# Kernel optimization log

Hardware: AMD Instinct MI355X
Metric: run time of the kernel (lower is better)

The kernel has to match this reference:

```python
import jax, jax.numpy as jnp
import numpy as np

B, Fch, H, W, K = 16, 6, 512, 512, 8
ITERS = 12
TEMP = 0.15
EPS = 1e-6


def setup_inputs() -> dict:
    key = jax.random.key(0)
    k1, k2 = jax.random.split(key)
    feat = jax.random.normal(k1, (B, Fch, H, W), dtype=jnp.float32)
    idx = jax.random.randint(k2, (B, K), 0, H * W)
    return {"feat": feat, "idx": idx}


def reference(feat, idx):
    Bn, F_, Hh, Ww = feat.shape
    N = Hh * Ww
    # (B,F,H,W) -> (B,N,F), per-channel standardize over pixels (torch std is unbiased)
    X = feat.reshape(Bn, F_, N).transpose(0, 2, 1)
    X = X - X.mean(axis=1, keepdims=True)
    X = X / jnp.clip(X.std(axis=1, keepdims=True, ddof=1), EPS, None)
    # initial centroids: gather K random pixels per batch
    C0 = jnp.take_along_axis(X, idx[:, :, None], axis=1)  # (B,K,F)
    x2 = jnp.sum(X * X, axis=2, keepdims=True)  # (B,N,1), loop-invariant

    def step(carry, _):
        C, _S = carry
        c2 = jnp.sum(C * C, axis=2)[:, None, :]            # (B,1,K)
        xc = jnp.einsum('bnf,bkf->bnk', X, C)              # (B,N,K)
        d2 = jnp.clip(x2 + c2 - 2.0 * xc, 0.0, None)
        S = jax.nn.softmax(-d2 / TEMP, axis=2)             # (B,N,K)
        denom = jnp.clip(S.sum(axis=1)[:, :, None], EPS, None)  # (B,K,1)
        Cn = jnp.einsum('bnk,bnf->bkf', S, X) / denom
        return (Cn, S), None

    S_init = jnp.zeros((Bn, N, K), dtype=feat.dtype)
    (_, S), _ = jax.lax.scan(step, (C0, S_init), None, length=ITERS)
    # last S (computed from centroids of the previous update), as in the torch loop
    S_img = S.transpose(0, 2, 1).reshape(Bn, K, Hh, Ww)
    S_img = S_img / jnp.clip(S_img.sum(axis=1, keepdims=True), EPS, None)
    return S_img
```

## Files before the change

kernel.cpp:

```cpp
#include <hip/hip_runtime.h>
#include <math.h>

#define Bn    16
#define FCH   6
#define NPIX  262144
#define KC    8
#define NITERS 12
#define EPSF  1e-6f
#define ALPHA2 19.235933878519512f

#if __has_builtin(__builtin_amdgcn_exp2f)
#define EXP2(x) __builtin_amdgcn_exp2f(x)
#else
#define EXP2(x) __expf((x) * 0.6931471805599453f)
#endif

#if __has_builtin(__builtin_amdgcn_rcpf)
#define RCPF(x) __builtin_amdgcn_rcpf(x)
#else
#define RCPF(x) (1.0f / (x))
#endif

#define WS_SCALE 0
#define WS_SHIFT 96
#define WS_C     192
#define WS_PART  2048
#define WS_PART2 5120
#define WS_ACC0  8192
#define ACCBUF_STRIDE 1024

#define TPB 256
#define PPT 32

__device__ __forceinline__ float rfl(float x) {
    return __int_as_float(__builtin_amdgcn_readfirstlane(__float_as_int(x)));
}

__global__ __launch_bounds__(256) void stats_partial(const float* __restrict__ feat,
                                                     float* __restrict__ ws) {
    const int bf = blockIdx.x >> 5;
    const int c  = blockIdx.x & 31;
    const float4* p = (const float4*)(feat + (size_t)bf * NPIX) + c * 2048;
    float s = 0.f, ss = 0.f;
    for (int i = threadIdx.x; i < 2048; i += 256) {
        float4 v = p[i];
        s  += v.x + v.y + v.z + v.w;
        ss += v.x * v.x + v.y * v.y + v.z * v.z + v.w * v.w;
    }
#pragma unroll
    for (int off = 32; off > 0; off >>= 1) {
        s  += __shfl_down(s,  off, 64);
        ss += __shfl_down(ss, off, 64);
    }
    __shared__ float sh[8];
    const int w = threadIdx.x >> 6;
    if ((threadIdx.x & 63) == 0) { sh[w] = s; sh[4 + w] = ss; }
    __syncthreads();
    if (threadIdx.x == 0) {
        s  = sh[0] + sh[1] + sh[2] + sh[3];
        ss = sh[4] + sh[5] + sh[6] + sh[7];
        ws[WS_PART  + blockIdx.x] = s;
        ws[WS_PART2 + blockIdx.x] = ss;
    }
}

__global__ void init_kernel(const float* __restrict__ feat,
                            const int* __restrict__ idx,
                            float* __restrict__ ws) {
    const int t = threadIdx.x;
    for (int i = t; i < ACCBUF_STRIDE; i += 128) ws[WS_ACC0 + i] = 0.f;
    if (t < Bn * FCH) {
        float s = 0.f, ss = 0.f;
        for (int c = 0; c < 32; ++c) {
            s  += ws[WS_PART  + t * 32 + c];
            ss += ws[WS_PART2 + t * 32 + c];
        }
        float mean = s / (float)NPIX;
        float var  = (ss - s * mean) / (float)(NPIX - 1);
        float sd   = sqrtf(fmaxf(var, 0.f));
        float scale = 1.f / fmaxf(sd, EPSF);
        ws[WS_SCALE + t] = scale;
        ws[WS_SHIFT + t] = -mean * scale;
    }
    __syncthreads();
    {
        const int b = t / KC;
        const int n = idx[t];
        for (int f = 0; f < FCH; ++f) {
            const int bf = b * FCH + f;
            float v = fmaf(feat[(size_t)bf * NPIX + n], ws[WS_SCALE + bf], ws[WS_SHIFT + bf]);
            ws[WS_C + t * FCH + f] = v;
        }
    }
}

template <int LAST>
__global__ __launch_bounds__(TPB, 2) void assign_kernel(const float* __restrict__ feat,
                                                        const float* __restrict__ ws,
                                                        float* __restrict__ out,
                                                        float* __restrict__ accAdd,
                                                        const float* __restrict__ accRead,
                                                        float* __restrict__ accZero,
                                                        const int first) {
    const int b = blockIdx.y;
    const int t = threadIdx.x;

    __shared__ float sWb[KC * FCH + KC];
    __shared__ float sBlk[KC * FCH + KC];

    if (t < KC) {
        float sc[FCH], sh[FCH], C[FCH];
#pragma unroll
        for (int f = 0; f < FCH; ++f) {
            sc[f] = ws[WS_SCALE + b * FCH + f];
            sh[f] = ws[WS_SHIFT + b * FCH + f];
        }
        if (first) {
#pragma unroll
            for (int f = 0; f < FCH; ++f) C[f] = ws[WS_C + (b * KC + t) * FCH + f];
        } else {
            float as  = accRead[b * 64 + 48 + t];
            float inv = 1.f / fmaxf(as, EPSF);
#pragma unroll
            for (int f = 0; f < FCH; ++f)
                C[f] = (sc[f] * accRead[b * 64 + t * FCH + f] + sh[f] * as) * inv;
        }
        float c2 = 0.f, sd = 0.f;
#pragma unroll
        for (int f = 0; f < FCH; ++f) {
            c2 = fmaf(C[f], C[f], c2);
            sd = fmaf(sh[f], C[f], sd);
            sWb[t * FCH + f] = ALPHA2 * sc[f] * C[f];
        }
        sWb[KC * FCH + t] = ALPHA2 * sd - 0.5f * ALPHA2 * c2;
    }
    if (!LAST) {
        if (t < KC * FCH + KC) sBlk[t] = 0.f;
        if (blockIdx.x == 0 && t < 64) accZero[b * 64 + t] = 0.f;
    }
    __syncthreads();

    float W[KC][FCH], bias[KC];
#pragma unroll
    for (int k = 0; k < KC; ++k) {
        bias[k] = rfl(sWb[KC * FCH + k]);
#pragma unroll
        for (int f = 0; f < FCH; ++f) W[k][f] = rfl(sWb[k * FCH + f]);
    }

    const float4* fb4 = (const float4*)(feat + (size_t)b * FCH * NPIX);
    const int base4 = blockIdx.x * (PPT * TPB / 4) + t;

    float accC[KC][FCH], accS[KC];
    if (!LAST) {
#pragma unroll
        for (int k = 0; k < KC; ++k) {
            accS[k] = 0.f;
#pragma unroll
            for (int f = 0; f < FCH; ++f) accC[k][f] = 0.f;
        }
    }

    float4 cur[FCH];
#pragma unroll
    for (int f = 0; f < FCH; ++f) cur[f] = fb4[f * (NPIX / 4) + base4];

    for (int j = 0; j < PPT / 4; ++j) {
        float4 nxt[FCH];
        {
            const int jn = (j + 1 < PPT / 4) ? (j + 1) : j;
            const int i4n = base4 + jn * TPB;
#pragma unroll
            for (int f = 0; f < FCH; ++f) nxt[f] = fb4[f * (NPIX / 4) + i4n];
        }

        float rr[FCH][4];
#pragma unroll
        for (int f = 0; f < FCH; ++f) {
            rr[f][0] = cur[f].x; rr[f][1] = cur[f].y; rr[f][2] = cur[f].z; rr[f][3] = cur[f].w;
        }
        float sv[KC][4];
#pragma unroll
        for (int px = 0; px < 4; ++px) {
            float l[KC];
#pragma unroll
            for (int k = 0; k < KC; ++k) {
                float v = bias[k];
#pragma unroll
                for (int f = 0; f < FCH; ++f) v = fmaf(rr[f][px], W[k][f], v);
                l[k] = v;
            }
            float m01 = fmaxf(l[0], l[1]), m23 = fmaxf(l[2], l[3]);
            float m45 = fmaxf(l[4], l[5]), m67 = fmaxf(l[6], l[7]);
            float m = fmaxf(fmaxf(m01, m23), fmaxf(m45, m67));
            float e[KC];
#pragma unroll
            for (int k = 0; k < KC; ++k) e[k] = EXP2(l[k] - m);
            float s01 = e[0] + e[1], s23 = e[2] + e[3];
            float s45 = e[4] + e[5], s67 = e[6] + e[7];
            float sum = (s01 + s23) + (s45 + s67);
            const float inv = RCPF(sum);
            if (LAST) {
#pragma unroll
                for (int k = 0; k < KC; ++k) sv[k][px] = e[k] * inv;
            } else {
#pragma unroll
                for (int k = 0; k < KC; ++k) {
                    float s = e[k] * inv;
                    accS[k] += s;
#pragma unroll
                    for (int f = 0; f < FCH; ++f) accC[k][f] = fmaf(s, rr[f][px], accC[k][f]);
                }
            }
        }
        if (LAST) {
            const int i4 = base4 + j * TPB;
            float4* out4 = (float4*)out;
#pragma unroll
            for (int k = 0; k < KC; ++k)
                out4[((size_t)(b * KC + k)) * (NPIX / 4) + i4] =
                    make_float4(sv[k][0], sv[k][1], sv[k][2], sv[k][3]);
        }

#pragma unroll
        for (int f = 0; f < FCH; ++f) cur[f] = nxt[f];
    }

    if (!LAST) {
#pragma unroll
        for (int k = 0; k < KC; ++k) {
#pragma unroll
            for (int off = 32; off > 0; off >>= 1) accS[k] += __shfl_down(accS[k], off, 64);
#pragma unroll
            for (int f = 0; f < FCH; ++f)
#pragma unroll
                for (int off = 32; off > 0; off >>= 1) accC[k][f] += __shfl_down(accC[k][f], off, 64);
        }
        if ((t & 63) == 0) {
#pragma unroll
            for (int k = 0; k < KC; ++k) {
                atomicAdd(&sBlk[KC * FCH + k], accS[k]);
#pragma unroll
                for (int f = 0; f < FCH; ++f) atomicAdd(&sBlk[k * FCH + f], accC[k][f]);
            }
        }
        __syncthreads();
        if (t < KC * FCH)
            atomicAdd(&accAdd[b * 64 + t], sBlk[t]);
        else if (t < KC * FCH + KC)
            atomicAdd(&accAdd[b * 64 + 48 + (t - KC * FCH)], sBlk[t]);
    }
}

extern "C" void kernel_launch(void* const* d_in, const int* in_sizes, int n_in,
                              void* d_out, int out_size, void* d_ws, size_t ws_size,
                              hipStream_t stream) {
    const float* feat = (const float*)d_in[0];
    const int*   idx  = (const int*)d_in[1];
    float* out = (float*)d_out;
    float* ws  = (float*)d_ws;

    stats_partial<<<Bn * FCH * 32, 256, 0, stream>>>(feat, ws);
    init_kernel<<<1, 128, 0, stream>>>(feat, idx, ws);

    dim3 grid(NPIX / (PPT * TPB), Bn);
    for (int it = 0; it < NITERS; ++it) {
        float*       bufA = ws + WS_ACC0 + (it % 3)       * ACCBUF_STRIDE;
        const float* bufR = ws + WS_ACC0 + ((it + 2) % 3) * ACCBUF_STRIDE;
        float*       bufZ = ws + WS_ACC0 + ((it + 1) % 3) * ACCBUF_STRIDE;
        if (it == NITERS - 1)
            assign_kernel<1><<<grid, TPB, 0, stream>>>(feat, ws, out, nullptr, bufR, nullptr, 0);
        else
            assign_kernel<0><<<grid, TPB, 0, stream>>>(feat, ws, out, bufA, bufR, bufZ, it == 0);
    }
}
```

Before: 547.5 us.

## Fuse all k-means passes into one persistent cooperative kernel with grid syncs

Replaces the sequence of stats, init and twelve assign-kernel launches with a single cooperative kernel of 512 blocks. The phases are separated by grid-wide barriers, and cross-block data goes through relaxed agent-scope atomics. The aim is to remove per-launch overhead and the gaps between the 14 launches. The cost is grid.sync barriers plus fences, and an occupancy limit of 2 blocks per CU. If the cooperative launch fails, the code falls back to the old multi-kernel path.

```diff
diff --git a/kernel.cpp b/kernel.cpp
--- a/kernel.cpp
+++ b/kernel.cpp
@@ -1,5 +1,8 @@
 #include <hip/hip_runtime.h>
+#include <hip/hip_cooperative_groups.h>
 #include <math.h>
+
+namespace cg = cooperative_groups;
 
 #define Bn    16
 #define FCH   6
@@ -31,9 +34,281 @@
 
 #define TPB 256
 #define PPT 32
+#define NBLK 512
 
 __device__ __forceinline__ float rfl(float x) {
     return __int_as_float(__builtin_amdgcn_readfirstlane(__float_as_int(x)));
+}
+
+__device__ __forceinline__ float ald(const float* p) {
+    return __hip_atomic_load(p, __ATOMIC_RELAXED, __HIP_MEMORY_SCOPE_AGENT);
+}
+__device__ __forceinline__ void ast(float* p, float v) {
+    __hip_atomic_store(p, v, __ATOMIC_RELAXED, __HIP_MEMORY_SCOPE_AGENT);
+}
+
+template <int LAST>
+__device__ __forceinline__ void pass_body(const float4* __restrict__ fb4,
+                                          float* __restrict__ out,
+                                          float* __restrict__ accAdd,
+                                          const float (&W)[KC][FCH],
+                                          const float (&bias)[KC],
+                                          float* __restrict__ sBlk,
+                                          const int b, const int bx, const int t) {
+    const int base4 = bx * (PPT * TPB / 4) + t;
+
+    float accC[KC][FCH], accS[KC];
+    if (!LAST) {
+#pragma unroll
+        for (int k = 0; k < KC; ++k) {
+            accS[k] = 0.f;
+#pragma unroll
+            for (int f = 0; f < FCH; ++f) accC[k][f] = 0.f;
+        }
+    }
+
+    float4 cur[FCH];
+#pragma unroll
+    for (int f = 0; f < FCH; ++f) cur[f] = fb4[f * (NPIX / 4) + base4];
+
+    for (int j = 0; j < PPT / 4; ++j) {
+        float4 nxt[FCH];
+        {
+            const int jn = (j + 1 < PPT / 4) ? (j + 1) : j;
+            const int i4n = base4 + jn * TPB;
+#pragma unroll
+            for (int f = 0; f < FCH; ++f) nxt[f] = fb4[f * (NPIX / 4) + i4n];
+        }
+
+        float rr[FCH][4];
+#pragma unroll
+        for (int f = 0; f < FCH; ++f) {
+            rr[f][0] = cur[f].x; rr[f][1] = cur[f].y; rr[f][2] = cur[f].z; rr[f][3] = cur[f].w;
+        }
+        float sv[KC][4];
+#pragma unroll
+        for (int px = 0; px < 4; ++px) {
+            float l[KC];
+#pragma unroll
+            for (int k = 0; k < KC; ++k) {
+                float v = bias[k];
+#pragma unroll
+                for (int f = 0; f < FCH; ++f) v = fmaf(rr[f][px], W[k][f], v);
+                l[k] = v;
+            }
+            float m01 = fmaxf(l[0], l[1]), m23 = fmaxf(l[2], l[3]);
+            float m45 = fmaxf(l[4], l[5]), m67 = fmaxf(l[6], l[7]);
+            float m = fmaxf(fmaxf(m01, m23), fmaxf(m45, m67));
+            float e[KC];
+#pragma unroll
+            for (int k = 0; k < KC; ++k) e[k] = EXP2(l[k] - m);
+            float s01 = e[0] + e[1], s23 = e[2] + e[3];
+            float s45 = e[4] + e[5], s67 = e[6] + e[7];
+            float sum = (s01 + s23) + (s45 + s67);
+            const float inv = RCPF(sum);
+            if (LAST) {
+#pragma unroll
+                for (int k = 0; k < KC; ++k) sv[k][px] = e[k] * inv;
+            } else {
+#pragma unroll
+                for (int k = 0; k < KC; ++k) {
+                    float s = e[k] * inv;
+                    accS[k] += s;
+#pragma unroll
+                    for (int f = 0; f < FCH; ++f) accC[k][f] = fmaf(s, rr[f][px], accC[k][f]);
+                }
+            }
+        }
+        if (LAST) {
+            const int i4 = base4 + j * TPB;
+            float4* out4 = (float4*)out;
+#pragma unroll
+            for (int k = 0; k < KC; ++k)
+                out4[((size_t)(b * KC + k)) * (NPIX / 4) + i4] =
+                    make_float4(sv[k][0], sv[k][1], sv[k][2], sv[k][3]);
+        }
+
+#pragma unroll
+        for (int f = 0; f < FCH; ++f) cur[f] = nxt[f];
+    }
+
+    if (!LAST) {
+#pragma unroll
+        for (int k = 0; k < KC; ++k) {
+#pragma unroll
+            for (int off = 32; off > 0; off >>= 1) accS[k] += __shfl_down(accS[k], off, 64);
+#pragma unroll
+            for (int f = 0; f < FCH; ++f)
+#pragma unroll
+                for (int off = 32; off > 0; off >>= 1) accC[k][f] += __shfl_down(accC[k][f], off, 64);
+        }
+        if ((t & 63) == 0) {
+#pragma unroll
+            for (int k = 0; k < KC; ++k) {
+                atomicAdd(&sBlk[KC * FCH + k], accS[k]);
+#pragma unroll
+                for (int f = 0; f < FCH; ++f) atomicAdd(&sBlk[k * FCH + f], accC[k][f]);
+            }
+        }
+        __syncthreads();
+        if (t < KC * FCH)
+            atomicAdd(&accAdd[b * 64 + t], sBlk[t]);
+        else if (t < KC * FCH + KC)
+            atomicAdd(&accAdd[b * 64 + 48 + (t - KC * FCH)], sBlk[t]);
+    }
+}
+
+__device__ __forceinline__ void build_Wb_coh(const float* __restrict__ ws,
+                                             const float* __restrict__ accRead,
+                                             float* __restrict__ sWb,
+                                             const int b, const int t, const int first) {
+    if (t < KC) {
+        float sc[FCH], sh[FCH], C[FCH];
+#pragma unroll
+        for (int f = 0; f < FCH; ++f) {
+            sc[f] = ald(&ws[WS_SCALE + b * FCH + f]);
+            sh[f] = ald(&ws[WS_SHIFT + b * FCH + f]);
+        }
+        if (first) {
+#pragma unroll
+            for (int f = 0; f < FCH; ++f) C[f] = ald(&ws[WS_C + (b * KC + t) * FCH + f]);
+        } else {
+            float as  = ald(&accRead[b * 64 + 48 + t]);
+            float inv = 1.f / fmaxf(as, EPSF);
+#pragma unroll
+            for (int f = 0; f < FCH; ++f)
+                C[f] = (sc[f] * ald(&accRead[b * 64 + t * FCH + f]) + sh[f] * as) * inv;
+        }
+        float c2 = 0.f, sd = 0.f;
+#pragma unroll
+        for (int f = 0; f < FCH; ++f) {
+            c2 = fmaf(C[f], C[f], c2);
+            sd = fmaf(sh[f], C[f], sd);
+            sWb[t * FCH + f] = ALPHA2 * sc[f] * C[f];
+        }
+        sWb[KC * FCH + t] = ALPHA2 * sd - 0.5f * ALPHA2 * c2;
+    }
+}
+
+__global__ __launch_bounds__(TPB, 2) void fused_kernel(const float* __restrict__ feat,
+                                                       const int* __restrict__ idx,
+                                                       float* __restrict__ out,
+                                                       float* __restrict__ ws) {
+    cg::grid_group grid = cg::this_grid();
+    const int bid = blockIdx.x;
+    const int t   = threadIdx.x;
+
+    __shared__ float shr[8];
+    __shared__ float sWb[KC * FCH + KC];
+    __shared__ float sBlk[KC * FCH + KC];
+
+    if (bid == 0)
+        for (int i = t; i < ACCBUF_STRIDE; i += TPB) ast(&ws[WS_ACC0 + i], 0.f);
+
+    for (int task = bid; task < Bn * FCH * 32; task += NBLK) {
+        const int bf = task >> 5;
+        const int c  = task & 31;
+        const float4* p = (const float4*)(feat + (size_t)bf * NPIX) + c * 2048;
+        float s = 0.f, ss = 0.f;
+        for (int i = t; i < 2048; i += TPB) {
+            float4 v = p[i];
+            s  += v.x + v.y + v.z + v.w;
+            ss += v.x * v.x + v.y * v.y + v.z * v.z + v.w * v.w;
+        }
+#pragma unroll
+        for (int off = 32; off > 0; off >>= 1) {
+            s  += __shfl_down(s,  off, 64);
+            ss += __shfl_down(ss, off, 64);
+        }
+        const int wv = t >> 6;
+        if ((t & 63) == 0) { shr[wv] = s; shr[4 + wv] = ss; }
+        __syncthreads();
+        if (t == 0) {
+            s  = shr[0] + shr[1] + shr[2] + shr[3];
+            ss = shr[4] + shr[5] + shr[6] + shr[7];
+            ast(&ws[WS_PART  + task], s);
+            ast(&ws[WS_PART2 + task], ss);
+        }
+        __syncthreads();
+    }
+    __threadfence();
+    grid.sync();
+    __threadfence();
+
+    if (bid == 0) {
+        if (t < Bn * FCH) {
+            float s = 0.f, ss = 0.f;
+            for (int c = 0; c < 32; ++c) {
+                s  += ald(&ws[WS_PART  + t * 32 + c]);
+                ss += ald(&ws[WS_PART2 + t * 32 + c]);
+            }
+            float mean = s / (float)NPIX;
+            float var  = (ss - s * mean) / (float)(NPIX - 1);
+            float sd   = sqrtf(fmaxf(var, 0.f));
+            float scale = 1.f / fmaxf(sd, EPSF);
+            ast(&ws[WS_SCALE + t], scale);
+            ast(&ws[WS_SHIFT + t], -mean * scale);
+        }
+        __syncthreads();
+        if (t < Bn * KC) {
+            const int b = t / KC;
+            const int n = idx[t];
+            for (int f = 0; f < FCH; ++f) {
+                const int bf = b * FCH + f;
+                float v = fmaf(feat[(size_t)bf * NPIX + n],
+                               ald(&ws[WS_SCALE + bf]), ald(&ws[WS_SHIFT + bf]));
+                ast(&ws[WS_C + t * FCH + f], v);
+            }
+        }
+    }
+    __threadfence();
+    grid.sync();
+    __threadfence();
+
+    const int b  = bid >> 5;
+    const int bx = bid & 31;
+    const float4* fb4 = (const float4*)(feat + (size_t)b * FCH * NPIX);
+
+    for (int it = 0; it < NITERS - 1; ++it) {
+        float*       bufA = ws + WS_ACC0 + (it % 3)       * ACCBUF_STRIDE;
+        const float* bufR = ws + WS_ACC0 + ((it + 2) % 3) * ACCBUF_STRIDE;
+        float*       bufZ = ws + WS_ACC0 + ((it + 1) % 3) * ACCBUF_STRIDE;
+
+        build_Wb_coh(ws, bufR, sWb, b, t, it == 0);
+        if (t < KC * FCH + KC) sBlk[t] = 0.f;
+        if (bx == 0 && t < 64) ast(&bufZ[b * 64 + t], 0.f);
+        __syncthreads();
+
+        float W[KC][FCH], bias[KC];
+#pragma unroll
+        for (int k = 0; k < KC; ++k) {
+            bias[k] = rfl(sWb[KC * FCH + k]);
+#pragma unroll
+            for (int f = 0; f < FCH; ++f) W[k][f] = rfl(sWb[k * FCH + f]);
+        }
+
+        pass_body<0>(fb4, out, bufA, W, bias, sBlk, b, bx, t);
+
+        __threadfence();
+        grid.sync();
+        __threadfence();
+    }
+
+    {
+        const float* bufR = ws + WS_ACC0 + ((NITERS - 1 + 2) % 3) * ACCBUF_STRIDE;
+        build_Wb_coh(ws, bufR, sWb, b, t, 0);
+        __syncthreads();
+
+        float W[KC][FCH], bias[KC];
+#pragma unroll
+        for (int k = 0; k < KC; ++k) {
+            bias[k] = rfl(sWb[KC * FCH + k]);
+#pragma unroll
+            for (int f = 0; f < FCH; ++f) W[k][f] = rfl(sWb[k * FCH + f]);
+        }
+
+        pass_body<1>(fb4, out, nullptr, W, bias, sBlk, b, bx, t);
+    }
 }
 
 __global__ __launch_bounds__(256) void stats_partial(const float* __restrict__ feat,
@@ -143,113 +418,13 @@
     float W[KC][FCH], bias[KC];
 #pragma unroll
     for (int k = 0; k < KC; ++k) {
-        bias[k] = rfl(sWb[KC * FCH + k]);
-#pragma unroll
-        for (int f = 0; f < FCH; ++f) W[k][f] = rfl(sWb[k * FCH + f]);
-    }
-
-    const float4* fb4 = (const float4*)(feat + (size_t)b * FCH * NPIX);
-    const int base4 = blockIdx.x * (PPT * TPB / 4) + t;
-
-    float accC[KC][FCH], accS[KC];
-    if (!LAST) {
-#pragma unroll
-        for (int k = 0; k < KC; ++k) {
-            accS[k] = 0.f;
-#pragma unroll
-            for (int f = 0; f < FCH; ++f) accC[k][f] = 0.f;
-        }
-    }
-
-    float4 cur[FCH];
-#pragma unroll
-    for (int f = 0; f < FCH; ++f) cur[f] = fb4[f * (NPIX / 4) + base4];
-
-    for (int j = 0; j < PPT / 4; ++j) {
-        float4 nxt[FCH];
-        {
-            const int jn = (j + 1 < PPT / 4) ? (j + 1) : j;
-            const int i4n = base4 + jn * TPB;
-#pragma unroll
-            for (int f = 0; f < FCH; ++f) nxt[f] = fb4[f * (NPIX / 4) + i4n];
-        }
-
-        float rr[FCH][4];
-#pragma unroll
-        for (int f = 0; f < FCH; ++f) {
-            rr[f][0] = cur[f].x; rr[f][1] = cur[f].y; rr[f][2] = cur[f].z; rr[f][3] = cur[f].w;
-        }
-        float sv[KC][4];
-#pragma unroll
-        for (int px = 0; px < 4; ++px) {
-            float l[KC];
-#pragma unroll
-            for (int k = 0; k < KC; ++k) {
-                float v = bias[k];
-#pragma unroll
-                for (int f = 0; f < FCH; ++f) v = fmaf(rr[f][px], W[k][f], v);
-                l[k] = v;
-            }
-            float m01 = fmaxf(l[0], l[1]), m23 = fmaxf(l[2], l[3]);
-            float m45 = fmaxf(l[4], l[5]), m67 = fmaxf(l[6], l[7]);
-            float m = fmaxf(fmaxf(m01, m23), fmaxf(m45, m67));
-            float e[KC];
-#pragma unroll
-            for (int k = 0; k < KC; ++k) e[k] = EXP2(l[k] - m);
-            float s01 = e[0] + e[1], s23 = e[2] + e[3];
-            float s45 = e[4] + e[5], s67 = e[6] + e[7];
-            float sum = (s01 + s23) + (s45 + s67);
-            const float inv = RCPF(sum);
-            if (LAST) {
-#pragma unroll
-                for (int k = 0; k < KC; ++k) sv[k][px] = e[k] * inv;
-            } else {
-#pragma unroll
-                for (int k = 0; k < KC; ++k) {
-                    float s = e[k] * inv;
-                    accS[k] += s;
-#pragma unroll
-                    for (int f = 0; f < FCH; ++f) accC[k][f] = fmaf(s, rr[f][px], accC[k][f]);
-                }
-            }
-        }
-        if (LAST) {
-            const int i4 = base4 + j * TPB;
-            float4* out4 = (float4*)out;
-#pragma unroll
-            for (int k = 0; k < KC; ++k)
-                out4[((size_t)(b * KC + k)) * (NPIX / 4) + i4] =
-                    make_float4(sv[k][0], sv[k][1], sv[k][2], sv[k][3]);
-        }
-
-#pragma unroll
-        for (int f = 0; f < FCH; ++f) cur[f] = nxt[f];
-    }
-
-    if (!LAST) {
-#pragma unroll
-        for (int k = 0; k < KC; ++k) {
-#pragma unroll
-            for (int off = 32; off > 0; off >>= 1) accS[k] += __shfl_down(accS[k], off, 64);
-#pragma unroll
-            for (int f = 0; f < FCH; ++f)
-#pragma unroll
-                for (int off = 32; off > 0; off >>= 1) accC[k][f] += __shfl_down(accC[k][f], off, 64);
-        }
-        if ((t & 63) == 0) {
-#pragma unroll
-            for (int k = 0; k < KC; ++k) {
-                atomicAdd(&sBlk[KC * FCH + k], accS[k]);
-#pragma unroll
-                for (int f = 0; f < FCH; ++f) atomicAdd(&sBlk[k * FCH + f], accC[k][f]);
-            }
-        }
-        __syncthreads();
-        if (t < KC * FCH)
-            atomicAdd(&accAdd[b * 64 + t], sBlk[t]);
-        else if (t < KC * FCH + KC)
-            atomicAdd(&accAdd[b * 64 + 48 + (t - KC * FCH)], sBlk[t]);
-    }
+        bias[k] = sWb[KC * FCH + k];
+#pragma unroll
+        for (int f = 0; f < FCH; ++f) W[k][f] = sWb[k * FCH + f];
+    }
+
+    pass_body<LAST>((const float4*)(feat + (size_t)b * FCH * NPIX), out,
+                    accAdd ? accAdd : (float*)nullptr, W, bias, sBlk, b, blockIdx.x, t);
 }
 
 extern "C" void kernel_launch(void* const* d_in, const int* in_sizes, int n_in,
@@ -259,6 +434,11 @@
     const int*   idx  = (const int*)d_in[1];
     float* out = (float*)d_out;
     float* ws  = (float*)d_ws;
+
+    void* args[] = {(void*)&feat, (void*)&idx, (void*)&out, (void*)&ws};
+    hipError_t err = hipLaunchCooperativeKernel((const void*)fused_kernel,
+                                                dim3(NBLK), dim3(TPB), args, 0, stream);
+    if (err == hipSuccess) return;
 
     stats_partial<<<Bn * FCH * 32, 256, 0, stream>>>(feat, ws);
     init_kernel<<<1, 128, 0, stream>>>(feat, idx, ws);
```

Result: slower. 1.910 ms (+248.8%).
